# Kernel optimization log

Hardware: AMD Instinct MI355X
Metric: run time of the kernel (lower is better)

## Reference

```python
import jax, jax.numpy as jnp
import numpy as np

N_PTILES = 4096
MAX_SOURCES = 1
PTILE_SLEN = 53  # odd -> slen == ptile_slen, size_lens is identity
N_BANDS = 1


def setup_inputs() -> dict:
    key = jax.random.key(0)
    k1, k2, k3, k4, k5, k6 = jax.random.split(key, 6)
    shape = (N_PTILES, MAX_SOURCES)
    gal = jax.random.uniform(k1, shape + (7,), dtype=jnp.float32)
    # realistic SIE lens params per _sample_lens_params: b in [5,30], q in (0,1)
    b = jax.random.uniform(k2, shape + (1,), dtype=jnp.float32) * 25.0 + 5.0
    centers = jax.random.normal(k3, shape + (2,), dtype=jnp.float32)
    q = jax.random.uniform(k4, shape + (1,), dtype=jnp.float32) * 0.8 + 0.1
    beta = (jax.random.uniform(k5, shape + (1,), dtype=jnp.float32) - 0.5) * (np.pi / 2)
    ellf = (1.0 - q) / (1.0 + q)
    e1 = ellf * jnp.cos(beta)
    e2 = ellf * jnp.sin(beta)
    lens_params = jnp.concatenate([gal, b, centers, e1, e2], axis=-1)  # [..., 12]
    bools = (jax.random.uniform(k6, shape + (1,), dtype=jnp.float32) < 0.7).astype(jnp.float32)
    return {"lens_params": lens_params, "lensed_galaxy_bools": bools}


def _render_unlensed(gal_p, slen):
    # Differentiable Gaussian stand-in for the (CPU galsim) unlensed source render.
    c = jnp.arange(slen, dtype=jnp.float32) - (slen - 1) / 2.0
    yy, xx = jnp.meshgrid(c, c, indexing="ij")
    flux = gal_p[:, 0] * 1000.0 + 100.0      # [N]
    sigma = gal_p[:, 3] * 3.0 + 1.0          # [N]
    r2 = xx[None] ** 2 + yy[None] ** 2       # [1, S, S]
    s2 = (sigma ** 2)[:, None, None]
    return flux[:, None, None] * jnp.exp(-0.5 * r2 / s2) / (2.0 * np.pi * s2)


def _sie_deflection(x, y, lens_p):
    # x, y: [1, S, S]; lens_p: [N, 5] -> (xg, yg): [N, S, S]
    b, cx, cy, e1, e2 = [lens_p[:, i][:, None, None] for i in range(5)]
    ell = jnp.sqrt(e1 ** 2 + e2 ** 2)
    q = (1.0 - ell) / (1.0 + ell)
    phirad = jnp.arctan(e2 / e1)
    cosp, sinp = jnp.cos(phirad), jnp.sin(phirad)
    xsie = (x - cx) * cosp + (y - cy) * sinp
    ysie = (y - cy) * cosp - (x - cx) * sinp
    r_ell = jnp.sqrt(q * xsie ** 2 + ysie ** 2 / q + 1e-12)
    qfact = jnp.sqrt(1.0 / q - q)
    eps = 0.001
    safe = jnp.maximum(qfact, eps)
    denom = r_ell + (r_ell == 0)
    xtg = jnp.where(qfact >= eps, b / safe * jnp.arctan(safe * xsie / denom), b * xsie / denom)
    ytg = jnp.where(qfact >= eps, b / safe * jnp.arctanh(safe * ysie / denom), b * ysie / denom)
    xg = xtg * cosp - ytg * sinp
    yg = ytg * cosp + xtg * sinp
    return xg, yg


def _bilinear(im, xs, ys):
    # im: [N, S, S]; xs (col coord), ys (row coord): [N, S, S]
    N, S, _ = im.shape
    x0 = jnp.clip(jnp.floor(xs).astype(jnp.int32), 0, S - 1)
    x1 = jnp.clip(jnp.floor(xs).astype(jnp.int32) + 1, 0, S - 1)
    y0 = jnp.clip(jnp.floor(ys).astype(jnp.int32), 0, S - 1)
    y1 = jnp.clip(jnp.floor(ys).astype(jnp.int32) + 1, 0, S - 1)
    flat = im.reshape(N, S * S)

    def g(yi, xi):
        return jnp.take_along_axis(flat, (yi * S + xi).reshape(N, -1), axis=1).reshape(N, S, S)

    x0f, x1f = x0.astype(im.dtype), x1.astype(im.dtype)
    y0f, y1f = y0.astype(im.dtype), y1.astype(im.dtype)
    # weights use the CLIPPED integer corners, matching bilinear_interpolate_numpy
    wa = (x1f - xs) * (y1f - ys)
    wb = (x1f - xs) * (ys - y0f)
    wc = (xs - x0f) * (y1f - ys)
    wd = (xs - x0f) * (ys - y0f)
    return g(y0, x0) * wa + g(y1, x0) * wb + g(y0, x1) * wc + g(y1, x1) * wd


def _forward(lens_params, lensed_galaxy_bools):
    n_ptiles, max_s, P = lens_params.shape
    z = lens_params.reshape(-1, P)
    gal_p, lens_p = z[:, :7], z[:, 7:]
    slen = PTILE_SLEN
    unlensed = _render_unlensed(gal_p, slen)            # [N, S, S]
    # grid exactly as lens_galsim: range [-nx//2, nx//2] over nx points
    nx = slen
    lo = float((-nx) // 2)   # -27 for nx=53
    hi = float(nx // 2)      # 26
    coords = (hi - lo) * jnp.arange(nx, dtype=jnp.float32) / (nx - 1) + lo
    x = jnp.broadcast_to(coords[None, :], (nx, nx))  # varies along columns
    y = jnp.broadcast_to(coords[:, None], (nx, nx))  # varies along rows
    xg, yg = _sie_deflection(x[None], y[None], lens_p)
    shift = float(nx // 2)
    lensed = _bilinear(unlensed, x[None] - xg + shift, y[None] - yg + shift)
    out = lensed.reshape(n_ptiles, max_s, N_BANDS, slen, slen)
    # render-all + mask is equivalent to the zeros-init + boolean-fill + final mask
    return out * lensed_galaxy_bools[..., None, None]


def reference(lens_params, lensed_galaxy_bools):
    return _forward(lens_params, lensed_galaxy_bools)
```

## Files before the change

### kernel.cpp

```cpp
#include <hip/hip_runtime.h>
#include <math.h>

#define SLEN 53
#define NPIX 2809
#define NPARAM 12
#define BLK 256
#define PW 16

__device__ __forceinline__ float fast_atan(float u) {
    float t = __builtin_fabsf(u);
    float rin = __builtin_amdgcn_rcpf(t);
    bool big = t > 1.0f;
    float w = big ? rin : t;
    float z = w * w;
    float p = -0.01172120f;
    p = __builtin_fmaf(p, z,  0.05265332f);
    p = __builtin_fmaf(p, z, -0.11643287f);
    p = __builtin_fmaf(p, z,  0.19354346f);
    p = __builtin_fmaf(p, z, -0.33262347f);
    p = __builtin_fmaf(p, z,  0.99997726f);
    float r = w * p;
    r = big ? 1.57079632679489662f - r : r;
    return __builtin_copysignf(r, u);
}

__device__ __forceinline__ float fast_atanh(float v) {
    float a = __builtin_fabsf(v);
    float t = (1.0f + a) * __builtin_amdgcn_rcpf(1.0f - a);
    float r = 0.34657359027997264f * __builtin_amdgcn_logf(t);
    return __builtin_copysignf(r, v);
}

__global__ __launch_bounds__(BLK) void prep_kernel(
    const float* __restrict__ lens_params,
    const float* __restrict__ bools,
    float* __restrict__ ws, int n_tiles)
{
    int t = blockIdx.x * blockDim.x + threadIdx.x;
    if (t >= n_tiles) return;
    const float* p = lens_params + t * NPARAM;
    const float bl   = bools[t];
    const float flux = p[0] * 1000.0f + 100.0f;
    const float sg   = p[3] * 3.0f + 1.0f;
    const float s2   = sg * sg;
    const float A    = bl * flux / (6.28318530717958647692f * s2);
    const float nh2  = -0.5f / s2 * 1.44269504088896340736f;
    const float b  = p[7], cx = p[8], cy = p[9], e1 = p[10], e2 = p[11];
    const float ell  = sqrtf(e1 * e1 + e2 * e2);
    const float q    = (1.0f - ell) / (1.0f + ell);
    const float qinv = 1.0f / q;
    const float ph   = atanf(e2 / e1);
    const float cosp = cosf(ph), sinp = sinf(ph);
    const float qf   = sqrtf(qinv - q);
    const float safe = fmaxf(qf, 0.001f);
    const float bos  = b / safe;
    float* w = ws + t * PW;
    w[0]  = bl;   w[1]  = A;    w[2]  = nh2;  w[3]  = cosp;
    w[4]  = sinp; w[5]  = q;    w[6]  = qinv; w[7]  = safe;
    w[8]  = bos;  w[9]  = cx;   w[10] = cy;   w[11] = b;
    w[12] = (qf >= 0.001f) ? 1.0f : 0.0f;
    w[13] = 0.0f; w[14] = 0.0f; w[15] = 0.0f;
}

template<bool MB>
__device__ __forceinline__ void run_tile(
    float* __restrict__ outp, int lane, int wv, const float* __restrict__ Etab,
    const float* __restrict__ Ctab,
    float A, float cosp, float sinp, float q, float qinv,
    float safe, float bos, float cx, float cy, float b)
{
    const float xcl  = Ctab[lane];
    const float dx   = xcl - cx;
    const float dxc  = dx * cosp;
    const float dxs  = dx * sinp;
    const float xc26 = xcl + 26.0f;

    for (int r = wv; r < SLEN; r += 4) {
        const float ycr  = Ctab[r];
        const float dy   = ycr - cy;
        const float t1   = dy * sinp;
        const float t2   = dy * cosp;
        const float yc26 = ycr + 26.0f;

        const float xsie = dxc + t1;
        const float ysie = t2 - dxs;
        const float arg  = __builtin_fmaf(q * xsie, xsie,
                           __builtin_fmaf(qinv * ysie, ysie, 1e-12f));
        const float rcp_r = __builtin_amdgcn_rsqf(arg);
        float xtg, ytg;
        if (MB) {
            xtg = bos * fast_atan(safe * xsie * rcp_r);
            ytg = bos * fast_atanh(safe * ysie * rcp_r);
        } else {
            xtg = b * xsie * rcp_r;
            ytg = b * ysie * rcp_r;
        }
        const float xg = xtg * cosp - ytg * sinp;
        const float yg = ytg * cosp + xtg * sinp;
        const float xs = xc26 - xg;
        const float ys = yc26 - yg;
        const float fx = __builtin_floorf(xs);
        const float fy = __builtin_floorf(ys);
        const float x0f = fminf(fmaxf(fx,        0.0f), 52.0f);
        const float x1f = fminf(fmaxf(fx + 1.0f, 0.0f), 52.0f);
        const float y0f = fminf(fmaxf(fy,        0.0f), 52.0f);
        const float y1f = fminf(fmaxf(fy + 1.0f, 0.0f), 52.0f);
        const int x0 = (int)x0f, x1 = (int)x1f;
        const int y0 = (int)y0f, y1 = (int)y1f;
        const float Fx = (x1f - xs) * Etab[x0] + (xs - x0f) * Etab[x1];
        const float Fy = (y1f - ys) * Etab[y0] + (ys - y0f) * Etab[y1];
        outp[r * SLEN + lane] = A * Fx * Fy;
    }
}

__global__ __launch_bounds__(BLK) void lgtd_kernel(
    const float* __restrict__ ws,
    float* __restrict__ out)
{
    const int tile = blockIdx.x;
    const float* w = ws + tile * PW;
    float* outp = out + (size_t)tile * NPIX;
    const int tid = threadIdx.x;

    const float bl = w[0];
    if (bl == 0.0f) {
        #pragma unroll
        for (int s = 0; s < 11; ++s) {
            const int idx = s * BLK + tid;
            if (s < 10 || idx < NPIX) outp[idx] = 0.0f;
        }
        return;
    }

    const float A    = w[1],  nh2  = w[2],  cosp = w[3], sinp = w[4];
    const float q    = w[5],  qinv = w[6],  safe = w[7], bos  = w[8];
    const float cx   = w[9],  cy   = w[10], b    = w[11];
    const bool  mb   = (w[12] != 0.0f);

    __shared__ float Ctab[SLEN];
    __shared__ float Etab[SLEN];
    if (tid < SLEN) {
        const float kf = (float)tid;
        Ctab[tid] = 53.0f * kf / 52.0f - 27.0f;
        const float d = kf - 26.0f;
        Etab[tid] = __builtin_amdgcn_exp2f(nh2 * (d * d));
    }
    __syncthreads();

    const int lane = tid & 63;
    const int wv   = tid >> 6;
    if (lane >= SLEN) return;

    if (mb)
        run_tile<true >(outp, lane, wv, Etab, Ctab, A, cosp, sinp, q, qinv, safe, bos, cx, cy, b);
    else
        run_tile<false>(outp, lane, wv, Etab, Ctab, A, cosp, sinp, q, qinv, safe, bos, cx, cy, b);
}

extern "C" void kernel_launch(void* const* d_in, const int* in_sizes, int n_in,
                              void* d_out, int out_size, void* d_ws, size_t ws_size,
                              hipStream_t stream) {
    const float* lens  = (const float*)d_in[0];
    const float* bools = (const float*)d_in[1];
    float* out = (float*)d_out;
    float* ws  = (float*)d_ws;
    const int n_tiles = in_sizes[1];
    prep_kernel<<<(n_tiles + BLK - 1) / BLK, BLK, 0, stream>>>(lens, bools, ws, n_tiles);
    lgtd_kernel<<<n_tiles, BLK, 0, stream>>>(ws, out);
}
```

Before: 87.94 us.

## Flatten pixel mapping across full block and recompute Gaussian weights inline

Replaces the row-per-wave mapping, which left 11 of 64 lanes idle per wave, with a flat pixel index spread over all 256 threads in 11 unrolled slots. Row and column come from a multiply-shift division by 53. The shared-memory coordinate and exponential tables and the block barrier are removed; each pixel now evaluates four exp2 calls and computes its coordinates directly. This trades extra transcendental arithmetic per pixel for full lane use, no LDS traffic and no synchronisation.

New measurement: 88.99 us. Within noise of the previous version (+1.2%).

```diff
diff --git a/kernel.cpp b/kernel.cpp
--- a/kernel.cpp
+++ b/kernel.cpp
@@ -6,6 +6,7 @@
 #define NPARAM 12
 #define BLK 256
 #define PW 16
+#define NSLOT 11
 
 __device__ __forceinline__ float fast_atan(float u) {
     float t = __builtin_fabsf(u);
@@ -64,26 +65,24 @@
 
 template<bool MB>
 __device__ __forceinline__ void run_tile(
-    float* __restrict__ outp, int lane, int wv, const float* __restrict__ Etab,
-    const float* __restrict__ Ctab,
-    float A, float cosp, float sinp, float q, float qinv,
+    float* __restrict__ outp, int tid,
+    float A, float nh2, float cosp, float sinp, float q, float qinv,
     float safe, float bos, float cx, float cy, float b)
 {
-    const float xcl  = Ctab[lane];
-    const float dx   = xcl - cx;
-    const float dxc  = dx * cosp;
-    const float dxs  = dx * sinp;
-    const float xc26 = xcl + 26.0f;
+    const float KC = 1.019230769230769231f;
+    #pragma unroll
+    for (int s = 0; s < NSLOT; ++s) {
+        const int idx = s * BLK + tid;
+        const bool ok = (s < NSLOT - 1) || (idx < NPIX);
+        const int idc = ok ? idx : NPIX - 1;
+        const unsigned i = ((unsigned)idc * 39569u) >> 21;
+        const int j = idc - (int)i * 53;
+        const float xc = __builtin_fmaf((float)j, KC, -27.0f);
+        const float yc = __builtin_fmaf((float)i, KC, -27.0f);
 
-    for (int r = wv; r < SLEN; r += 4) {
-        const float ycr  = Ctab[r];
-        const float dy   = ycr - cy;
-        const float t1   = dy * sinp;
-        const float t2   = dy * cosp;
-        const float yc26 = ycr + 26.0f;
-
-        const float xsie = dxc + t1;
-        const float ysie = t2 - dxs;
+        const float dx = xc - cx, dy = yc - cy;
+        const float xsie = __builtin_fmaf(dx, cosp, dy * sinp);
+        const float ysie = __builtin_fmaf(dy, cosp, -dx * sinp);
         const float arg  = __builtin_fmaf(q * xsie, xsie,
                            __builtin_fmaf(qinv * ysie, ysie, 1e-12f));
         const float rcp_r = __builtin_amdgcn_rsqf(arg);
@@ -95,21 +94,29 @@
             xtg = b * xsie * rcp_r;
             ytg = b * ysie * rcp_r;
         }
-        const float xg = xtg * cosp - ytg * sinp;
-        const float yg = ytg * cosp + xtg * sinp;
-        const float xs = xc26 - xg;
-        const float ys = yc26 - yg;
+        const float xg = __builtin_fmaf(xtg, cosp, -ytg * sinp);
+        const float yg = __builtin_fmaf(ytg, cosp,  xtg * sinp);
+
+        const float xs = (xc + 26.0f) - xg;
+        const float ys = (yc + 26.0f) - yg;
         const float fx = __builtin_floorf(xs);
         const float fy = __builtin_floorf(ys);
         const float x0f = fminf(fmaxf(fx,        0.0f), 52.0f);
         const float x1f = fminf(fmaxf(fx + 1.0f, 0.0f), 52.0f);
         const float y0f = fminf(fmaxf(fy,        0.0f), 52.0f);
         const float y1f = fminf(fmaxf(fy + 1.0f, 0.0f), 52.0f);
-        const int x0 = (int)x0f, x1 = (int)x1f;
-        const int y0 = (int)y0f, y1 = (int)y1f;
-        const float Fx = (x1f - xs) * Etab[x0] + (xs - x0f) * Etab[x1];
-        const float Fy = (y1f - ys) * Etab[y0] + (ys - y0f) * Etab[y1];
-        outp[r * SLEN + lane] = A * Fx * Fy;
+
+        const float dx0 = x0f - 26.0f, dx1 = x1f - 26.0f;
+        const float dy0 = y0f - 26.0f, dy1 = y1f - 26.0f;
+        const float Ex0 = __builtin_amdgcn_exp2f((nh2 * dx0) * dx0);
+        const float Ex1 = __builtin_amdgcn_exp2f((nh2 * dx1) * dx1);
+        const float Ey0 = __builtin_amdgcn_exp2f((nh2 * dy0) * dy0);
+        const float Ey1 = __builtin_amdgcn_exp2f((nh2 * dy1) * dy1);
+
+        const float Fx = __builtin_fmaf(x1f - xs, Ex0, (xs - x0f) * Ex1);
+        const float Fy = __builtin_fmaf(y1f - ys, Ey0, (ys - y0f) * Ey1);
+        const float val = A * Fx * Fy;
+        if (ok) outp[idx] = val;
     }
 }
 
@@ -125,9 +132,9 @@
     const float bl = w[0];
     if (bl == 0.0f) {
         #pragma unroll
-        for (int s = 0; s < 11; ++s) {
+        for (int s = 0; s < NSLOT; ++s) {
             const int idx = s * BLK + tid;
-            if (s < 10 || idx < NPIX) outp[idx] = 0.0f;
+            if (s < NSLOT - 1 || idx < NPIX) outp[idx] = 0.0f;
         }
         return;
     }
@@ -135,26 +142,11 @@
     const float A    = w[1],  nh2  = w[2],  cosp = w[3], sinp = w[4];
     const float q    = w[5],  qinv = w[6],  safe = w[7], bos  = w[8];
     const float cx   = w[9],  cy   = w[10], b    = w[11];
-    const bool  mb   = (w[12] != 0.0f);
 
-    __shared__ float Ctab[SLEN];
-    __shared__ float Etab[SLEN];
-    if (tid < SLEN) {
-        const float kf = (float)tid;
-        Ctab[tid] = 53.0f * kf / 52.0f - 27.0f;
-        const float d = kf - 26.0f;
-        Etab[tid] = __builtin_amdgcn_exp2f(nh2 * (d * d));
-    }
-    __syncthreads();
-
-    const int lane = tid & 63;
-    const int wv   = tid >> 6;
-    if (lane >= SLEN) return;
-
-    if (mb)
-        run_tile<true >(outp, lane, wv, Etab, Ctab, A, cosp, sinp, q, qinv, safe, bos, cx, cy, b);
+    if (w[12] != 0.0f)
+        run_tile<true >(outp, tid, A, nh2, cosp, sinp, q, qinv, safe, bos, cx, cy, b);
     else
-        run_tile<false>(outp, lane, wv, Etab, Ctab, A, cosp, sinp, q, qinv, safe, bos, cx, cy, b);
+        run_tile<false>(outp, tid, A, nh2, cosp, sinp, q, qinv, safe, bos, cx, cy, b);
 }
 
 extern "C" void kernel_launch(void* const* d_in, const int* in_sizes, int n_in,
```
